# Performance work log

Measured on AMD Instinct MI355X. Metric: run time of the kernel, lower is better.

Reference implementation:

```python
import jax, jax.numpy as jnp
import numpy as np

D_MODEL, D_K, D_V = 512, 64, 64
LN_EPS = 1e-6


def setup_inputs() -> dict:
    key = jax.random.key(0)
    ks = jax.random.split(key, 8)
    B, Lq, Lk = 2, 1024, 1024
    q = jax.random.normal(ks[0], (B, Lq, D_MODEL), dtype=jnp.float32)
    k = jax.random.normal(ks[1], (B, Lk, D_MODEL), dtype=jnp.float32)
    v = jax.random.normal(ks[2], (B, Lk, D_MODEL), dtype=jnp.float32)
    s = 1.0 / np.sqrt(D_MODEL)
    Wq = jax.random.normal(ks[3], (D_MODEL, D_K), dtype=jnp.float32) * s
    Wk = jax.random.normal(ks[4], (D_MODEL, D_K), dtype=jnp.float32) * s
    Wv = jax.random.normal(ks[5], (D_MODEL, D_V), dtype=jnp.float32) * s
    v_param = jax.random.normal(ks[6], (D_K,), dtype=jnp.float32)
    Wfc = jax.random.normal(ks[7], (D_V, D_MODEL), dtype=jnp.float32) / np.sqrt(D_V)
    ln_gamma = jnp.ones((D_MODEL,), dtype=jnp.float32)
    ln_beta = jnp.zeros((D_MODEL,), dtype=jnp.float32)
    return {"q": q, "k": k, "v": v, "Wq": Wq, "Wk": Wk, "Wv": Wv,
            "v_param": v_param, "Wfc": Wfc, "ln_gamma": ln_gamma, "ln_beta": ln_beta}


def reference(q, k, v, Wq, Wk, Wv, v_param, Wfc, ln_gamma, ln_beta):
    residual = q
    qp = q @ Wq                      # [B, Lq, d_k]
    kp = k @ Wk                      # [B, Lk, d_k]
    vp = v @ Wv                      # [B, Lk, d_v]
    # additive (Bahdanau) scores: tanh(q_i + k_j) . v_param  -> [B, Lq, Lk]
    scores = jnp.einsum("bqkd,d->bqk", jnp.tanh(qp[:, :, None, :] + kp[:, None, :, :]), v_param)
    attn = jax.nn.softmax(scores, axis=-1)   # dropout is identity in eval mode
    out = jnp.einsum("bqk,bkv->bqv", attn, vp)
    out = out @ Wfc + residual               # [B, Lq, d_model]
    mu = jnp.mean(out, axis=-1, keepdims=True)
    var = jnp.var(out, axis=-1, keepdims=True)
    out = (out - mu) * jax.lax.rsqrt(var + LN_EPS) * ln_gamma + ln_beta
    return out, attn
```

## Files before the change

### kernel.cpp

```cpp
#include <hip/hip_runtime.h>
#include <cstddef>
#include <cstdint>

#define D_MODEL 512
#define DK 64
#define LQ 1024
#define LK 1024
#define NB 2
#define LN_EPS 1e-6f
#define L2E2 2.8853900817779268f

#define PR_ROWS 16
__global__ __launch_bounds__(256, 4) void proj_kernel(
    const float* __restrict__ q, const float* __restrict__ k,
    const float* __restrict__ v, const float* __restrict__ Wq,
    const float* __restrict__ Wk, const float* __restrict__ Wv,
    const float* __restrict__ v_param, float4* __restrict__ ab4,
    float2* __restrict__ ekT2, float* __restrict__ vp) {
  __shared__ float rows[PR_ROWS][D_MODEL];
  const int tid = threadIdx.x;
  const int type = blockIdx.x >> 7;
  const int r0 = (blockIdx.x & 127) * PR_ROWS;
  const float* __restrict__ in = (type == 0) ? q : (type == 1) ? k : v;
  const float* __restrict__ W = (type == 0) ? Wq : (type == 1) ? Wk : Wv;
  {
    const float4* __restrict__ in4 = (const float4*)(in + (size_t)r0 * D_MODEL);
    float4* r4 = (float4*)&rows[0][0];
#pragma unroll
    for (int t = 0; t < 8; ++t) r4[tid + 256 * t] = in4[tid + 256 * t];
  }
  __syncthreads();
  const int lane = tid & 63;
  const int wv = tid >> 6;
  const int rglob = r0 + wv * 4;
  const float* __restrict__ Wl = W + lane;
  float c0[4] = {0.f, 0.f, 0.f, 0.f}, c1[4] = {0.f, 0.f, 0.f, 0.f};
#pragma unroll 4
  for (int e = 0; e < D_MODEL; e += 4) {
    float w0 = Wl[(size_t)(e + 0) * DK];
    float w1 = Wl[(size_t)(e + 1) * DK];
    float w2 = Wl[(size_t)(e + 2) * DK];
    float w3 = Wl[(size_t)(e + 3) * DK];
#pragma unroll
    for (int r = 0; r < 4; ++r) {
      float4 x = *(const float4*)&rows[wv * 4 + r][e];
      c0[r] = fmaf(x.x, w0, c0[r]);
      c1[r] = fmaf(x.y, w1, c1[r]);
      c0[r] = fmaf(x.z, w2, c0[r]);
      c1[r] = fmaf(x.w, w3, c1[r]);
    }
  }
  float acc[4];
#pragma unroll
  for (int r = 0; r < 4; ++r) acc[r] = c0[r] + c1[r];
  if (type == 0) {
    float vpar = v_param[lane];
#pragma unroll
    for (int r = 0; r < 4; ++r) {
      float iv = __builtin_amdgcn_exp2f(-L2E2 * acc[r]);
      float A = vpar * iv, B = iv;
      float Ah = __shfl_down(A, 32);
      float Bh = __shfl_down(B, 32);
      if (lane < 32)
        ab4[(size_t)(rglob + r) * 32 + lane] = make_float4(A, B, Ah, Bh);
    }
  } else if (type == 1) {
    float e4[4], h4[4];
#pragma unroll
    for (int r = 0; r < 4; ++r) {
      e4[r] = __builtin_amdgcn_exp2f(L2E2 * acc[r]);
      h4[r] = __shfl_down(e4[r], 32);
    }
    if (lane < 32) {
      int b = rglob >> 10, j0 = rglob & 1023;
      float2* bp = ekT2 + (size_t)b * 32 * LK + (size_t)lane * LK + j0;
      *(float4*)bp = make_float4(e4[0], h4[0], e4[1], h4[1]);
      *(float4*)(bp + 2) = make_float4(e4[2], h4[2], e4[3], h4[3]);
    }
  } else {
#pragma unroll
    for (int r = 0; r < 4; ++r) vp[(size_t)(rglob + r) * DK + lane] = acc[r];
  }
}

#define RB 2
__global__ __launch_bounds__(256, 6) void attn_kernel(
    const float4* __restrict__ ab4, const float2* __restrict__ ekT2,
    const float* __restrict__ vp, const float* __restrict__ resid,
    const float* __restrict__ Wfc, const float* __restrict__ gamma,
    const float* __restrict__ beta, float* __restrict__ out,
    float* __restrict__ attn_out) {
  __shared__ float sc[RB][LK];
  __shared__ float4 pvred[4][RB][16];
  __shared__ __align__(16) float ovlT[DK][RB];
  __shared__ float red[2][RB][4];
  __shared__ float mred[RB][4], sred[RB][4];
  const int tid = threadIdx.x;
  const int row0 = blockIdx.x * RB;
  const int batch = row0 >> 10;
  const float2* __restrict__ ekT_b = ekT2 + (size_t)batch * 32 * LK;
  const float* __restrict__ vp_b = vp + (size_t)batch * LK * DK;
  const float4* __restrict__ abr0 = ab4 + (size_t)(row0 + 0) * 32;
  const float4* __restrict__ abr1 = ab4 + (size_t)(row0 + 1) * 32;

  float a0[4] = {0.f, 0.f, 0.f, 0.f};
  float a1[4] = {0.f, 0.f, 0.f, 0.f};

#pragma unroll
  for (int qd = 0; qd < 16; ++qd) {
    const float4* e0 =
        (const float4*)(ekT_b + (size_t)(2 * qd + 0) * LK + 4 * tid);
    const float4* e1 =
        (const float4*)(ekT_b + (size_t)(2 * qd + 1) * LK + 4 * tid);
    float4 ka = e0[0], kb = e0[1];
    float4 kc = e1[0], kd = e1[1];
    float2 k0[4], k1[4];
    k0[0] = make_float2(ka.x, ka.y); k0[1] = make_float2(ka.z, ka.w);
    k0[2] = make_float2(kb.x, kb.y); k0[3] = make_float2(kb.z, kb.w);
    k1[0] = make_float2(kc.x, kc.y); k1[1] = make_float2(kc.z, kc.w);
    k1[2] = make_float2(kd.x, kd.y); k1[3] = make_float2(kd.z, kd.w);
    float4 P0 = abr0[2 * qd], Q0 = abr0[2 * qd + 1];
    float4 P1 = abr1[2 * qd], Q1 = abr1[2 * qd + 1];
#pragma unroll
    for (int jj = 0; jj < 4; ++jj) {
#define QUAD(PP, QQ, ACC)                                                  \
  {                                                                        \
    float x1 = k0[jj].x + PP.y, x2 = k0[jj].y + PP.w;                      \
    float x3 = k1[jj].x + QQ.y, x4 = k1[jj].y + QQ.w;                      \
    float p12 = x1 * x2, p34 = x3 * x4;                                    \
    float n12 = fmaf(PP.z, x1, PP.x * x2);                                 \
    float n34 = fmaf(QQ.z, x3, QQ.x * x4);                                 \
    float num = fmaf(n34, p12, n12 * p34);                                 \
    ACC[jj] = fmaf(num, __builtin_amdgcn_rcpf(p12 * p34), ACC[jj]);        \
  }
      QUAD(P0, Q0, a0)
      QUAD(P1, Q1, a1)
#undef QUAD
    }
  }

  const int wave = __builtin_amdgcn_readfirstlane(tid >> 6);
  const int lane = tid & 63;

  {
    float pm0 = fminf(fminf(a0[0], a0[1]), fminf(a0[2], a0[3]));
    float pm1 = fminf(fminf(a1[0], a1[1]), fminf(a1[2], a1[3]));
#pragma unroll
    for (int off = 32; off > 0; off >>= 1) {
      pm0 = fminf(pm0, __shfl_xor(pm0, off));
      pm1 = fminf(pm1, __shfl_xor(pm1, off));
    }
    if (lane == 0) {
      mred[0][wave] = pm0;
      mred[1][wave] = pm1;
    }
    __syncthreads();
    float m0 = fminf(fminf(mred[0][0], mred[0][1]), fminf(mred[0][2], mred[0][3]));
    float m1 = fminf(fminf(mred[1][0], mred[1][1]), fminf(mred[1][2], mred[1][3]));
    float s0 = 0.f, s1 = 0.f;
#pragma unroll
    for (int jj = 0; jj < 4; ++jj) {
      a0[jj] = __builtin_amdgcn_exp2f((m0 - a0[jj]) * L2E2); s0 += a0[jj];
      a1[jj] = __builtin_amdgcn_exp2f((m1 - a1[jj]) * L2E2); s1 += a1[jj];
    }
#pragma unroll
    for (int off = 32; off > 0; off >>= 1) {
      s0 += __shfl_xor(s0, off);
      s1 += __shfl_xor(s1, off);
    }
    if (lane == 0) {
      sred[0][wave] = s0;
      sred[1][wave] = s1;
    }
    __syncthreads();
    float i0 = __builtin_amdgcn_rcpf(sred[0][0] + sred[0][1] + sred[0][2] + sred[0][3]);
    float i1 = __builtin_amdgcn_rcpf(sred[1][0] + sred[1][1] + sred[1][2] + sred[1][3]);
    float4 p0 = make_float4(a0[0] * i0, a0[1] * i0, a0[2] * i0, a0[3] * i0);
    float4 p1 = make_float4(a1[0] * i1, a1[1] * i1, a1[2] * i1, a1[3] * i1);
    *(float4*)&sc[0][4 * tid] = p0;
    *(float4*)&sc[1][4 * tid] = p1;
    *(float4*)(attn_out + (size_t)(row0 + 0) * LK + 4 * tid) = p0;
    *(float4*)(attn_out + (size_t)(row0 + 1) * LK + 4 * tid) = p1;
  }
  __syncthreads();

  {
    const int jj = lane >> 4, l16 = lane & 15;
    const float4* __restrict__ vp4 = (const float4*)vp_b;
    float4 a[RB];
#pragma unroll
    for (int r = 0; r < RB; ++r) a[r] = make_float4(0.f, 0.f, 0.f, 0.f);
#pragma unroll 4
    for (int it = 0; it < 64; ++it) {
      int j = (wave << 8) + (it << 2) + jj;
      float4 vv = vp4[(size_t)j * (DK / 4) + l16];
#pragma unroll
      for (int r = 0; r < RB; ++r) {
        float pw = sc[r][j];
        a[r].x = fmaf(pw, vv.x, a[r].x);
        a[r].y = fmaf(pw, vv.y, a[r].y);
        a[r].z = fmaf(pw, vv.z, a[r].z);
        a[r].w = fmaf(pw, vv.w, a[r].w);
      }
    }
#pragma unroll
    for (int r = 0; r < RB; ++r) {
      a[r].x += __shfl_xor(a[r].x, 16); a[r].y += __shfl_xor(a[r].y, 16);
      a[r].z += __shfl_xor(a[r].z, 16); a[r].w += __shfl_xor(a[r].w, 16);
      a[r].x += __shfl_xor(a[r].x, 32); a[r].y += __shfl_xor(a[r].y, 32);
      a[r].z += __shfl_xor(a[r].z, 32); a[r].w += __shfl_xor(a[r].w, 32);
    }
    if (jj == 0) {
#pragma unroll
      for (int r = 0; r < RB; ++r) pvred[wave][r][l16] = a[r];
    }
  }
  __syncthreads();
  if (tid < 32) {
    int r = tid >> 4, l16 = tid & 15;
    float4 s = make_float4(0.f, 0.f, 0.f, 0.f);
#pragma unroll
    for (int w = 0; w < 4; ++w) {
      float4 t = pvred[w][r][l16];
      s.x += t.x; s.y += t.y; s.z += t.z; s.w += t.w;
    }
    ovlT[l16 * 4 + 0][r] = s.x;
    ovlT[l16 * 4 + 1][r] = s.y;
    ovlT[l16 * 4 + 2][r] = s.z;
    ovlT[l16 * 4 + 3][r] = s.w;
  }
  __syncthreads();

  {
    const int c0 = tid, c1 = tid + 256;
    float y[RB][2];
#pragma unroll
    for (int r = 0; r < RB; ++r) {
      y[r][0] = resid[(size_t)(row0 + r) * D_MODEL + c0];
      y[r][1] = resid[(size_t)(row0 + r) * D_MODEL + c1];
    }
#pragma unroll 4
    for (int e = 0; e < DK; ++e) {
      float w0 = Wfc[(size_t)e * D_MODEL + c0];
      float w1 = Wfc[(size_t)e * D_MODEL + c1];
      float2 ov = *(const float2*)&ovlT[e][0];
      y[0][0] = fmaf(ov.x, w0, y[0][0]); y[0][1] = fmaf(ov.x, w1, y[0][1]);
      y[1][0] = fmaf(ov.y, w0, y[1][0]); y[1][1] = fmaf(ov.y, w1, y[1][1]);
    }
#pragma unroll
    for (int r = 0; r < RB; ++r) {
      float s = y[r][0] + y[r][1];
#pragma unroll
      for (int off = 32; off > 0; off >>= 1) s += __shfl_xor(s, off);
      if (lane == 0) red[0][r][wave] = s;
    }
    __syncthreads();
    float mu[RB];
#pragma unroll
    for (int r = 0; r < RB; ++r)
      mu[r] = (red[0][r][0] + red[0][r][1] + red[0][r][2] + red[0][r][3]) *
              (1.0f / D_MODEL);
#pragma unroll
    for (int r = 0; r < RB; ++r) {
      float d0 = y[r][0] - mu[r], d1 = y[r][1] - mu[r];
      float s = d0 * d0 + d1 * d1;
#pragma unroll
      for (int off = 32; off > 0; off >>= 1) s += __shfl_xor(s, off);
      if (lane == 0) red[1][r][wave] = s;
    }
    __syncthreads();
    float g0 = gamma[c0], g1 = gamma[c1], b0 = beta[c0], b1 = beta[c1];
#pragma unroll
    for (int r = 0; r < RB; ++r) {
      float var = (red[1][r][0] + red[1][r][1] + red[1][r][2] + red[1][r][3]) *
                  (1.0f / D_MODEL);
      float rstd = rsqrtf(var + LN_EPS);
      out[(size_t)(row0 + r) * D_MODEL + c0] = (y[r][0] - mu[r]) * rstd * g0 + b0;
      out[(size_t)(row0 + r) * D_MODEL + c1] = (y[r][1] - mu[r]) * rstd * g1 + b1;
    }
  }
}

extern "C" void kernel_launch(void* const* d_in, const int* in_sizes, int n_in,
                              void* d_out, int out_size, void* d_ws,
                              size_t ws_size, hipStream_t stream) {
  const float* q = (const float*)d_in[0];
  const float* k = (const float*)d_in[1];
  const float* v = (const float*)d_in[2];
  const float* Wq = (const float*)d_in[3];
  const float* Wk = (const float*)d_in[4];
  const float* Wv = (const float*)d_in[5];
  const float* v_param = (const float*)d_in[6];
  const float* Wfc = (const float*)d_in[7];
  const float* gamma = (const float*)d_in[8];
  const float* beta = (const float*)d_in[9];

  float* out = (float*)d_out;
  float* attn = out + (size_t)NB * LQ * D_MODEL;

  float* base = (float*)d_ws;
  float4* ab4 = (float4*)base;
  float* p1 = base + (size_t)NB * LQ * 32 * 4;
  float2* ekT2 = (float2*)p1;
  float* vp = p1 + (size_t)NB * 32 * LK * 2;

  hipLaunchKernelGGL(proj_kernel, dim3(3 * 128), dim3(256), 0, stream, q, k, v,
                     Wq, Wk, Wv, v_param, ab4, ekT2, vp);
  hipLaunchKernelGGL(attn_kernel, dim3(NB * LQ / RB), dim3(256), 0, stream,
                     ab4, ekT2, vp, q, Wfc, gamma, beta, out, attn);
}
```

Measured before the change: 55.21 us.

## Restructure projection kernel: per-thread 4-column tiles, smaller blocks, LDS-staged outputs

The projection kernel now gives each thread one input row and four adjacent output columns, reading the weights as float4 instead of scalar strided loads. Blocks shrink to 128 threads over 8 rows, so the grid doubles to 768 blocks. Outputs are staged through shared memory and then written in the interleaved ab4/ekT2 layouts with a block barrier. The goal is more parallelism and wider weight loads in the small projection stage. In exchange, each weight element is reused across fewer rows per thread and an extra sync is added.

```diff
diff --git a/kernel.cpp b/kernel.cpp
--- a/kernel.cpp
+++ b/kernel.cpp
@@ -10,76 +10,86 @@
 #define LN_EPS 1e-6f
 #define L2E2 2.8853900817779268f
 
-#define PR_ROWS 16
-__global__ __launch_bounds__(256, 4) void proj_kernel(
+#define PR_ROWS 8
+__global__ __launch_bounds__(128, 4) void proj_kernel(
     const float* __restrict__ q, const float* __restrict__ k,
     const float* __restrict__ v, const float* __restrict__ Wq,
     const float* __restrict__ Wk, const float* __restrict__ Wv,
     const float* __restrict__ v_param, float4* __restrict__ ab4,
     float2* __restrict__ ekT2, float* __restrict__ vp) {
   __shared__ float rows[PR_ROWS][D_MODEL];
+  __shared__ float stA[PR_ROWS][DK];
+  __shared__ float stB[PR_ROWS][DK];
   const int tid = threadIdx.x;
-  const int type = blockIdx.x >> 7;
-  const int r0 = (blockIdx.x & 127) * PR_ROWS;
+  const int type = blockIdx.x >> 8;
+  const int r0 = (blockIdx.x & 255) * PR_ROWS;
   const float* __restrict__ in = (type == 0) ? q : (type == 1) ? k : v;
   const float* __restrict__ W = (type == 0) ? Wq : (type == 1) ? Wk : Wv;
   {
     const float4* __restrict__ in4 = (const float4*)(in + (size_t)r0 * D_MODEL);
     float4* r4 = (float4*)&rows[0][0];
 #pragma unroll
-    for (int t = 0; t < 8; ++t) r4[tid + 256 * t] = in4[tid + 256 * t];
+    for (int t = 0; t < 8; ++t) r4[tid + 128 * t] = in4[tid + 128 * t];
   }
   __syncthreads();
-  const int lane = tid & 63;
-  const int wv = tid >> 6;
-  const int rglob = r0 + wv * 4;
-  const float* __restrict__ Wl = W + lane;
-  float c0[4] = {0.f, 0.f, 0.f, 0.f}, c1[4] = {0.f, 0.f, 0.f, 0.f};
+  const int r = tid >> 4;
+  const int qd = tid & 15;
+  const float4* __restrict__ W4 = (const float4*)W;
+  float4 a0 = make_float4(0.f, 0.f, 0.f, 0.f);
+  float4 a1 = make_float4(0.f, 0.f, 0.f, 0.f);
 #pragma unroll 4
   for (int e = 0; e < D_MODEL; e += 4) {
-    float w0 = Wl[(size_t)(e + 0) * DK];
-    float w1 = Wl[(size_t)(e + 1) * DK];
-    float w2 = Wl[(size_t)(e + 2) * DK];
-    float w3 = Wl[(size_t)(e + 3) * DK];
-#pragma unroll
-    for (int r = 0; r < 4; ++r) {
-      float4 x = *(const float4*)&rows[wv * 4 + r][e];
-      c0[r] = fmaf(x.x, w0, c0[r]);
-      c1[r] = fmaf(x.y, w1, c1[r]);
-      c0[r] = fmaf(x.z, w2, c0[r]);
-      c1[r] = fmaf(x.w, w3, c1[r]);
-    }
-  }
-  float acc[4];
-#pragma unroll
-  for (int r = 0; r < 4; ++r) acc[r] = c0[r] + c1[r];
-  if (type == 0) {
-    float vpar = v_param[lane];
-#pragma unroll
-    for (int r = 0; r < 4; ++r) {
-      float iv = __builtin_amdgcn_exp2f(-L2E2 * acc[r]);
-      float A = vpar * iv, B = iv;
-      float Ah = __shfl_down(A, 32);
-      float Bh = __shfl_down(B, 32);
-      if (lane < 32)
-        ab4[(size_t)(rglob + r) * 32 + lane] = make_float4(A, B, Ah, Bh);
-    }
-  } else if (type == 1) {
-    float e4[4], h4[4];
-#pragma unroll
-    for (int r = 0; r < 4; ++r) {
-      e4[r] = __builtin_amdgcn_exp2f(L2E2 * acc[r]);
-      h4[r] = __shfl_down(e4[r], 32);
-    }
-    if (lane < 32) {
-      int b = rglob >> 10, j0 = rglob & 1023;
-      float2* bp = ekT2 + (size_t)b * 32 * LK + (size_t)lane * LK + j0;
-      *(float4*)bp = make_float4(e4[0], h4[0], e4[1], h4[1]);
-      *(float4*)(bp + 2) = make_float4(e4[2], h4[2], e4[3], h4[3]);
+    float4 x = *(const float4*)&rows[r][e];
+    float4 w0 = W4[(size_t)(e + 0) * 16 + qd];
+    float4 w1 = W4[(size_t)(e + 1) * 16 + qd];
+    float4 w2 = W4[(size_t)(e + 2) * 16 + qd];
+    float4 w3 = W4[(size_t)(e + 3) * 16 + qd];
+    a0.x = fmaf(x.x, w0.x, a0.x); a0.y = fmaf(x.x, w0.y, a0.y);
+    a0.z = fmaf(x.x, w0.z, a0.z); a0.w = fmaf(x.x, w0.w, a0.w);
+    a1.x = fmaf(x.y, w1.x, a1.x); a1.y = fmaf(x.y, w1.y, a1.y);
+    a1.z = fmaf(x.y, w1.z, a1.z); a1.w = fmaf(x.y, w1.w, a1.w);
+    a0.x = fmaf(x.z, w2.x, a0.x); a0.y = fmaf(x.z, w2.y, a0.y);
+    a0.z = fmaf(x.z, w2.z, a0.z); a0.w = fmaf(x.z, w2.w, a0.w);
+    a1.x = fmaf(x.w, w3.x, a1.x); a1.y = fmaf(x.w, w3.y, a1.y);
+    a1.z = fmaf(x.w, w3.z, a1.z); a1.w = fmaf(x.w, w3.w, a1.w);
+  }
+  float4 acc = make_float4(a0.x + a1.x, a0.y + a1.y, a0.z + a1.z, a0.w + a1.w);
+  const int c0 = qd * 4;
+  if (type == 2) {
+    *(float4*)&vp[(size_t)(r0 + r) * DK + c0] = acc;
+  } else if (type == 0) {
+    float4 vp4 = *(const float4*)&v_param[c0];
+    float i0 = __builtin_amdgcn_exp2f(-L2E2 * acc.x);
+    float i1 = __builtin_amdgcn_exp2f(-L2E2 * acc.y);
+    float i2 = __builtin_amdgcn_exp2f(-L2E2 * acc.z);
+    float i3 = __builtin_amdgcn_exp2f(-L2E2 * acc.w);
+    stA[r][c0 + 0] = vp4.x * i0; stB[r][c0 + 0] = i0;
+    stA[r][c0 + 1] = vp4.y * i1; stB[r][c0 + 1] = i1;
+    stA[r][c0 + 2] = vp4.z * i2; stB[r][c0 + 2] = i2;
+    stA[r][c0 + 3] = vp4.w * i3; stB[r][c0 + 3] = i3;
+    __syncthreads();
+#pragma unroll
+    for (int s = 0; s < 2; ++s) {
+      int ent = tid + 128 * s;
+      int row = ent >> 5, dp = ent & 31;
+      ab4[(size_t)(r0 + row) * 32 + dp] =
+          make_float4(stA[row][dp], stB[row][dp],
+                      stA[row][dp + 32], stB[row][dp + 32]);
     }
   } else {
-#pragma unroll
-    for (int r = 0; r < 4; ++r) vp[(size_t)(rglob + r) * DK + lane] = acc[r];
+    stA[r][c0 + 0] = __builtin_amdgcn_exp2f(L2E2 * acc.x);
+    stA[r][c0 + 1] = __builtin_amdgcn_exp2f(L2E2 * acc.y);
+    stA[r][c0 + 2] = __builtin_amdgcn_exp2f(L2E2 * acc.z);
+    stA[r][c0 + 3] = __builtin_amdgcn_exp2f(L2E2 * acc.w);
+    __syncthreads();
+    const int b = r0 >> 10, j0 = r0 & 1023;
+#pragma unroll
+    for (int s = 0; s < 2; ++s) {
+      int ent = tid + 128 * s;
+      int dp = ent >> 3, jj = ent & 7;
+      ekT2[(size_t)b * 32 * LK + (size_t)dp * LK + j0 + jj] =
+          make_float2(stA[jj][dp], stA[jj][dp + 32]);
+    }
   }
 }
 
@@ -304,7 +314,7 @@
   float2* ekT2 = (float2*)p1;
   float* vp = p1 + (size_t)NB * 32 * LK * 2;
 
-  hipLaunchKernelGGL(proj_kernel, dim3(3 * 128), dim3(256), 0, stream, q, k, v,
+  hipLaunchKernelGGL(proj_kernel, dim3(3 * 256), dim3(128), 0, stream, q, k, v,
                      Wq, Wk, Wv, v_param, ab4, ekT2, vp);
   hipLaunchKernelGGL(attn_kernel, dim3(NB * LQ / RB), dim3(256), 0, stream,
                      ab4, ekT2, vp, q, Wfc, gamma, beta, out, attn);
```

After: 63.08 us. +14.3%, slower.
